# Optimization experiments

Hardware: AMD Instinct MI355X
Metric: run time of the kernel (lower is better)

The kernel has to match this reference:

```python
import jax, jax.numpy as jnp
import numpy as np

VOCAB, D, PATCH, ROUNDS = 256, 64, 4, 3
B, T = 32, 8192


def setup_inputs() -> dict:
    key = jax.random.key(0)
    ks = jax.random.split(key, 16)
    s = 0.02
    inp = {
        "x": jax.random.randint(ks[0], (B, T), 0, VOCAB),
        "emb": jax.random.normal(ks[1], (VOCAB, D), jnp.float32) * s,
        # msg_net: Linear(2d->d), GELU, Linear(d->d); weights stored [in, out]
        "w_m1": jax.random.normal(ks[2], (2 * D, D), jnp.float32) * s,
        "b_m1": jnp.zeros((D,), jnp.float32),
        "w_m2": jax.random.normal(ks[3], (D, D), jnp.float32) * s,
        "b_m2": jnp.zeros((D,), jnp.float32),
        # update_net: Linear(2d->d), GELU, Linear(d->d)
        "w_u1": jax.random.normal(ks[4], (2 * D, D), jnp.float32) * s,
        "b_u1": jnp.zeros((D,), jnp.float32),
        "w_u2": jax.random.normal(ks[5], (D, D), jnp.float32) * s,
        "b_u2": jnp.zeros((D,), jnp.float32),
        # LayerNorm(d)
        "ln_g": jnp.ones((D,), jnp.float32),
        "ln_b": jnp.zeros((D,), jnp.float32),
        # readout: Linear(d -> vocab)
        "w_r": jax.random.normal(ks[6], (D, VOCAB), jnp.float32) * s,
        "b_r": jnp.zeros((VOCAB,), jnp.float32),
    }
    return inp


def _mlp(z, w1, b1, w2, b2):
    h = jax.nn.gelu(z @ w1 + b1, approximate=False)  # torch nn.GELU default = exact erf
    return h @ w2 + b2


def _layernorm(h, g, b, eps=1e-5):
    mu = jnp.mean(h, axis=-1, keepdims=True)
    var = jnp.mean((h - mu) ** 2, axis=-1, keepdims=True)
    return (h - mu) / jnp.sqrt(var + eps) * g + b


def reference(x, emb, w_m1, b_m1, w_m2, b_m2, w_u1, b_u1, w_u2, b_u2, ln_g, ln_b, w_r, b_r):
    Bx, Tx = x.shape
    P = PATCH
    N = (Tx + P - 1) // P
    xp = jnp.pad(x, ((0, 0), (0, N * P - Tx)))  # pad token id 0
    h = emb[xp].reshape(Bx, N, P, D).mean(axis=2)  # [B, N, d] patch-node features
    for _ in range(ROUNDS):
        left = jnp.pad(h[:, :-1], ((0, 0), (1, 0), (0, 0)))  # shift-right along N
        msgs = _mlp(jnp.concatenate([h, left], axis=-1), w_m1, b_m1, w_m2, b_m2)
        upd = _mlp(jnp.concatenate([h, msgs], axis=-1), w_u1, b_u1, w_u2, b_u2)
        h = _layernorm(h + upd, ln_g, ln_b)
    tok = jnp.repeat(h, P, axis=1)[:, :Tx]  # broadcast node feat to its P tokens
    return tok @ w_r + b_r  # [B, T, vocab]
```

## Files before the change

kernel.cpp:

```cpp
#include <hip/hip_runtime.h>
#include <hip/hip_bf16.h>
#include <math.h>

#define DD 64
#define NPB 2048
#define RTOT 65536

typedef __bf16 bf16;
typedef bf16 bf16x8 __attribute__((ext_vector_type(8)));
typedef float f32x4 __attribute__((ext_vector_type(4)));
typedef short short4v __attribute__((ext_vector_type(4)));

#define COMPILER_FENCE() asm volatile("" ::: "memory")

__device__ __forceinline__ f32x4 mfma16(bf16x8 a, bf16x8 b, f32x4 c) {
  return __builtin_amdgcn_mfma_f32_16x16x32_bf16(a, b, c, 0, 0, 0);
}

__device__ __forceinline__ float gelu_fast(float x) {
  float u = fabsf(x) * 0.70710678118654752f;
  float t = __builtin_amdgcn_rcpf(fmaf(0.3275911f, u, 1.0f));
  float p = t * fmaf(t, fmaf(t, fmaf(t, fmaf(t, 1.061405429f, -1.453152027f),
                                     1.421413741f), -0.284496736f), 0.254829592f);
  float e = __expf(-u * u);
  float erfa = fmaf(-p, e, 1.0f);
  float s = copysignf(erfa, x);
  return 0.5f * x * (1.0f + s);
}

__device__ __forceinline__ int swz(int col, int row) {
  return col ^ ((row & 7) << 3);
}

__device__ __forceinline__ bf16x8 ld8(const bf16* p) {
  return *reinterpret_cast<const bf16x8*>(p);
}

__global__ void __launch_bounds__(256) k_pe(const int* __restrict__ x,
                                            const float* __restrict__ emb,
                                            const float* __restrict__ wm1,
                                            const float* __restrict__ wm2,
                                            const float* __restrict__ wu1,
                                            const float* __restrict__ wu2,
                                            const float* __restrict__ wr,
                                            bf16* __restrict__ Wsc,
                                            bf16* __restrict__ h) {
  const int b = blockIdx.x;
  if (b < 160) {
    int gid = b * 256 + threadIdx.x;
    if (gid < 8192) {
      int n = gid >> 7, k = gid & 127;
      Wsc[gid] = (bf16)wm1[k * 64 + n];
    } else if (gid < 16384) {
      int j = gid - 8192, n = j >> 7, k = j & 127;
      Wsc[gid] = (bf16)wu1[k * 64 + n];
    } else if (gid < 20480) {
      int j = gid - 16384, n = j >> 6, k = j & 63;
      Wsc[gid] = (bf16)wm2[k * 64 + n];
    } else if (gid < 24576) {
      int j = gid - 20480, n = j >> 6, k = j & 63;
      Wsc[gid] = (bf16)wu2[k * 64 + n];
    } else {
      int j = gid - 24576, v = j >> 6, k = j & 63;
      Wsc[gid] = (bf16)wr[k * 256 + v];
    }
  } else {
    int gid = (b - 160) * 256 + threadIdx.x;
    int row = gid >> 4, d0 = (gid & 15) * 4;
    const int* xp = x + row * 4;
    f32x4 s = {0.f, 0.f, 0.f, 0.f};
#pragma unroll
    for (int p = 0; p < 4; ++p)
      s += *reinterpret_cast<const f32x4*>(emb + xp[p] * DD + d0);
    short4v o;
#pragma unroll
    for (int j = 0; j < 4; ++j)
      o[j] = (short)__builtin_bit_cast(unsigned short, (bf16)(s[j] * 0.25f));
    *reinterpret_cast<short4v*>(h + row * DD + d0) = o;
  }
}

__global__ void __launch_bounds__(256) k_r(const bf16* __restrict__ hin,
                                           bf16* __restrict__ hout,
                                           const bf16* __restrict__ Wsc,
                                           const float* __restrict__ bm1,
                                           const float* __restrict__ bm2,
                                           const float* __restrict__ bu1,
                                           const float* __restrict__ bu2,
                                           const float* __restrict__ lng,
                                           const float* __restrict__ lnb) {
  __shared__ bf16 W1[2][64 * 128];
  __shared__ bf16 Ms[64 * 64];
  __shared__ bf16 Hs[64 * 64];

  const int tid = threadIdx.x;
  const int lane = tid & 63;
  const int wv = tid >> 6;
  const int l15 = lane & 15;
  const int lhi = lane >> 4;

  for (int i = tid; i < 2048; i += 256) {
    int buf = i >> 10, idx = i & 1023;
    int n = idx >> 4, g = (idx & 15) * 8;
    *reinterpret_cast<bf16x8*>(&W1[buf][n * 128 + swz(g, n)]) =
        ld8(Wsc + buf * 8192 + n * 128 + g);
  }
  bf16x8 fm2[4][2], fu2[4][2];
#pragma unroll
  for (int ct = 0; ct < 4; ++ct)
#pragma unroll
    for (int kt = 0; kt < 2; ++kt) {
      int off = (ct * 16 + l15) * 64 + kt * 32 + lhi * 8;
      fm2[ct][kt] = ld8(Wsc + 16384 + off);
      fu2[ct][kt] = ld8(Wsc + 20480 + off);
    }
  float bm1v[4], bm2v[4], bu1v[4], bu2v[4], lngv[4], lnbv[4];
#pragma unroll
  for (int ct = 0; ct < 4; ++ct) {
    int c = ct * 16 + l15;
    bm1v[ct] = bm1[c]; bm2v[ct] = bm2[c];
    bu1v[ct] = bu1[c]; bu2v[ct] = bu2[c];
    lngv[ct] = lng[c]; lnbv[ct] = lnb[c];
  }
  __syncthreads();

  const int lrow = wv * 16 + l15;
  const int sxr = (lrow & 7) << 3;
  const int sxw = (l15 & 7) << 3;
  const f32x4 fz = {0.f, 0.f, 0.f, 0.f};

  for (int tt = 0; tt < 2; ++tt) {
    const int rowbase = (blockIdx.x * 2 + tt) * 64;
    const int grow = rowbase + lrow;
    const bf16* hrow = hin + (size_t)grow * DD;

    bf16x8 ah0 = ld8(hrow + lhi * 8);
    bf16x8 ah1 = ld8(hrow + 32 + lhi * 8);
    bf16x8 al0, al1;
#pragma unroll
    for (int j = 0; j < 8; ++j) { al0[j] = (bf16)0.f; al1[j] = (bf16)0.f; }
    if ((grow & (NPB - 1)) != 0) {
      al0 = ld8(hrow - DD + lhi * 8);
      al1 = ld8(hrow - DD + 32 + lhi * 8);
    }

    f32x4 acc[4];
#pragma unroll
    for (int ct = 0; ct < 4; ++ct) acc[ct] = fz;
#pragma unroll
    for (int ct = 0; ct < 4; ++ct) {
      const bf16* wb = &W1[0][(ct * 16 + l15) * 128];
      acc[ct] = mfma16(ah0, ld8(wb + ((lhi * 8) ^ sxw)), acc[ct]);
      acc[ct] = mfma16(ah1, ld8(wb + ((32 + lhi * 8) ^ sxw)), acc[ct]);
      acc[ct] = mfma16(al0, ld8(wb + ((64 + lhi * 8) ^ sxw)), acc[ct]);
      acc[ct] = mfma16(al1, ld8(wb + ((96 + lhi * 8) ^ sxw)), acc[ct]);
    }
#pragma unroll
    for (int ct = 0; ct < 4; ++ct)
#pragma unroll
      for (int r = 0; r < 4; ++r) {
        float g = gelu_fast(acc[ct][r] + bm1v[ct]);
        int row = wv * 16 + lhi * 4 + r;
        Hs[row * 64 + swz(ct * 16 + l15, row)] = (bf16)g;
      }
    COMPILER_FENCE();
#pragma unroll
    for (int ct = 0; ct < 4; ++ct) acc[ct] = fz;
    {
      bf16x8 g0 = ld8(&Hs[lrow * 64 + ((lhi * 8) ^ sxr)]);
      bf16x8 g1 = ld8(&Hs[lrow * 64 + ((32 + lhi * 8) ^ sxr)]);
#pragma unroll
      for (int ct = 0; ct < 4; ++ct) {
        acc[ct] = mfma16(g0, fm2[ct][0], acc[ct]);
        acc[ct] = mfma16(g1, fm2[ct][1], acc[ct]);
      }
    }
#pragma unroll
    for (int ct = 0; ct < 4; ++ct)
#pragma unroll
      for (int r = 0; r < 4; ++r) {
        int row = wv * 16 + lhi * 4 + r;
        Ms[row * 64 + swz(ct * 16 + l15, row)] = (bf16)(acc[ct][r] + bm2v[ct]);
      }
    COMPILER_FENCE();
#pragma unroll
    for (int ct = 0; ct < 4; ++ct) acc[ct] = fz;
    {
      bf16x8 m0 = ld8(&Ms[lrow * 64 + ((lhi * 8) ^ sxr)]);
      bf16x8 m1 = ld8(&Ms[lrow * 64 + ((32 + lhi * 8) ^ sxr)]);
#pragma unroll
      for (int ct = 0; ct < 4; ++ct) {
        const bf16* wb = &W1[1][(ct * 16 + l15) * 128];
        acc[ct] = mfma16(ah0, ld8(wb + ((lhi * 8) ^ sxw)), acc[ct]);
        acc[ct] = mfma16(ah1, ld8(wb + ((32 + lhi * 8) ^ sxw)), acc[ct]);
        acc[ct] = mfma16(m0, ld8(wb + ((64 + lhi * 8) ^ sxw)), acc[ct]);
        acc[ct] = mfma16(m1, ld8(wb + ((96 + lhi * 8) ^ sxw)), acc[ct]);
      }
    }
    COMPILER_FENCE();
#pragma unroll
    for (int ct = 0; ct < 4; ++ct)
#pragma unroll
      for (int r = 0; r < 4; ++r) {
        float g = gelu_fast(acc[ct][r] + bu1v[ct]);
        int row = wv * 16 + lhi * 4 + r;
        Hs[row * 64 + swz(ct * 16 + l15, row)] = (bf16)g;
      }
    COMPILER_FENCE();
#pragma unroll
    for (int ct = 0; ct < 4; ++ct) acc[ct] = fz;
    {
      bf16x8 u0 = ld8(&Hs[lrow * 64 + ((lhi * 8) ^ sxr)]);
      bf16x8 u1 = ld8(&Hs[lrow * 64 + ((32 + lhi * 8) ^ sxr)]);
#pragma unroll
      for (int ct = 0; ct < 4; ++ct) {
        acc[ct] = mfma16(u0, fu2[ct][0], acc[ct]);
        acc[ct] = mfma16(u1, fu2[ct][1], acc[ct]);
      }
    }
    float xv[4][4];
#pragma unroll
    for (int ct = 0; ct < 4; ++ct)
#pragma unroll
      for (int r = 0; r < 4; ++r) {
        int row = rowbase + wv * 16 + lhi * 4 + r;
        xv[ct][r] = acc[ct][r] + bu2v[ct] + (float)hin[(size_t)row * DD + ct * 16 + l15];
      }
    float s1[4], s2[4];
#pragma unroll
    for (int r = 0; r < 4; ++r) {
      s1[r] = 0.f; s2[r] = 0.f;
#pragma unroll
      for (int ct = 0; ct < 4; ++ct) { s1[r] += xv[ct][r]; s2[r] += xv[ct][r] * xv[ct][r]; }
    }
#pragma unroll
    for (int off = 1; off < 16; off <<= 1)
#pragma unroll
      for (int r = 0; r < 4; ++r) {
        s1[r] += __shfl_xor(s1[r], off);
        s2[r] += __shfl_xor(s2[r], off);
      }
#pragma unroll
    for (int r = 0; r < 4; ++r) {
      float mu = s1[r] * 0.015625f;
      float var = s2[r] * 0.015625f - mu * mu;
      float rstd = rsqrtf(var + 1e-5f);
      int row = rowbase + wv * 16 + lhi * 4 + r;
#pragma unroll
      for (int ct = 0; ct < 4; ++ct)
        hout[(size_t)row * DD + ct * 16 + l15] =
            (bf16)((xv[ct][r] - mu) * rstd * lngv[ct] + lnbv[ct]);
    }
  }
}

__global__ void __launch_bounds__(256) k_r3r(const bf16* __restrict__ hin,
                                             const bf16* __restrict__ Wsc,
                                             const float* __restrict__ bm1,
                                             const float* __restrict__ bm2,
                                             const float* __restrict__ bu1,
                                             const float* __restrict__ bu2,
                                             const float* __restrict__ lng,
                                             const float* __restrict__ lnb,
                                             const float* __restrict__ br,
                                             float* __restrict__ out) {
  __shared__ bf16 W1[2][64 * 128];
  __shared__ bf16 Ms[64 * 64];
  __shared__ bf16 Hs[64 * 64];

  const int tid = threadIdx.x;
  const int lane = tid & 63;
  const int wv = tid >> 6;
  const int l15 = lane & 15;
  const int lhi = lane >> 4;

  for (int i = tid; i < 2048; i += 256) {
    int buf = i >> 10, idx = i & 1023;
    int n = idx >> 4, g = (idx & 15) * 8;
    *reinterpret_cast<bf16x8*>(&W1[buf][n * 128 + swz(g, n)]) =
        ld8(Wsc + buf * 8192 + n * 128 + g);
  }
  bf16x8 fm2[4][2], fu2[4][2];
#pragma unroll
  for (int ct = 0; ct < 4; ++ct)
#pragma unroll
    for (int kt = 0; kt < 2; ++kt) {
      int off = (ct * 16 + l15) * 64 + kt * 32 + lhi * 8;
      fm2[ct][kt] = ld8(Wsc + 16384 + off);
      fu2[ct][kt] = ld8(Wsc + 20480 + off);
    }
  const bf16* wrt = Wsc + 24576;
  float bm1v[4], bm2v[4], bu1v[4], bu2v[4], lngv[4], lnbv[4];
#pragma unroll
  for (int ct = 0; ct < 4; ++ct) {
    int c = ct * 16 + l15;
    bm1v[ct] = bm1[c]; bm2v[ct] = bm2[c];
    bu1v[ct] = bu1[c]; bu2v[ct] = bu2[c];
    lngv[ct] = lng[c]; lnbv[ct] = lnb[c];
  }
  __syncthreads();

  const int lrow = wv * 16 + l15;
  const int sxr = (lrow & 7) << 3;
  const int sxw = (l15 & 7) << 3;
  const f32x4 fz = {0.f, 0.f, 0.f, 0.f};

  for (int tt = 0; tt < 2; ++tt) {
    const int rowbase = (blockIdx.x * 2 + tt) * 64;
    const int grow = rowbase + lrow;
    const bf16* hrow = hin + (size_t)grow * DD;

    bf16x8 ah0 = ld8(hrow + lhi * 8);
    bf16x8 ah1 = ld8(hrow + 32 + lhi * 8);
    bf16x8 al0, al1;
#pragma unroll
    for (int j = 0; j < 8; ++j) { al0[j] = (bf16)0.f; al1[j] = (bf16)0.f; }
    if ((grow & (NPB - 1)) != 0) {
      al0 = ld8(hrow - DD + lhi * 8);
      al1 = ld8(hrow - DD + 32 + lhi * 8);
    }

    f32x4 acc[4];
#pragma unroll
    for (int ct = 0; ct < 4; ++ct) acc[ct] = fz;
#pragma unroll
    for (int ct = 0; ct < 4; ++ct) {
      const bf16* wb = &W1[0][(ct * 16 + l15) * 128];
      acc[ct] = mfma16(ah0, ld8(wb + ((lhi * 8) ^ sxw)), acc[ct]);
      acc[ct] = mfma16(ah1, ld8(wb + ((32 + lhi * 8) ^ sxw)), acc[ct]);
      acc[ct] = mfma16(al0, ld8(wb + ((64 + lhi * 8) ^ sxw)), acc[ct]);
      acc[ct] = mfma16(al1, ld8(wb + ((96 + lhi * 8) ^ sxw)), acc[ct]);
    }
#pragma unroll
    for (int ct = 0; ct < 4; ++ct)
#pragma unroll
      for (int r = 0; r < 4; ++r) {
        float g = gelu_fast(acc[ct][r] + bm1v[ct]);
        int row = wv * 16 + lhi * 4 + r;
        Hs[row * 64 + swz(ct * 16 + l15, row)] = (bf16)g;
      }
    COMPILER_FENCE();
#pragma unroll
    for (int ct = 0; ct < 4; ++ct) acc[ct] = fz;
    {
      bf16x8 g0 = ld8(&Hs[lrow * 64 + ((lhi * 8) ^ sxr)]);
      bf16x8 g1 = ld8(&Hs[lrow * 64 + ((32 + lhi * 8) ^ sxr)]);
#pragma unroll
      for (int ct = 0; ct < 4; ++ct) {
        acc[ct] = mfma16(g0, fm2[ct][0], acc[ct]);
        acc[ct] = mfma16(g1, fm2[ct][1], acc[ct]);
      }
    }
#pragma unroll
    for (int ct = 0; ct < 4; ++ct)
#pragma unroll
      for (int r = 0; r < 4; ++r) {
        int row = wv * 16 + lhi * 4 + r;
        Ms[row * 64 + swz(ct * 16 + l15, row)] = (bf16)(acc[ct][r] + bm2v[ct]);
      }
    COMPILER_FENCE();
#pragma unroll
    for (int ct = 0; ct < 4; ++ct) acc[ct] = fz;
    {
      bf16x8 m0 = ld8(&Ms[lrow * 64 + ((lhi * 8) ^ sxr)]);
      bf16x8 m1 = ld8(&Ms[lrow * 64 + ((32 + lhi * 8) ^ sxr)]);
#pragma unroll
      for (int ct = 0; ct < 4; ++ct) {
        const bf16* wb = &W1[1][(ct * 16 + l15) * 128];
        acc[ct] = mfma16(ah0, ld8(wb + ((lhi * 8) ^ sxw)), acc[ct]);
        acc[ct] = mfma16(ah1, ld8(wb + ((32 + lhi * 8) ^ sxw)), acc[ct]);
        acc[ct] = mfma16(m0, ld8(wb + ((64 + lhi * 8) ^ sxw)), acc[ct]);
        acc[ct] = mfma16(m1, ld8(wb + ((96 + lhi * 8) ^ sxw)), acc[ct]);
      }
    }
    COMPILER_FENCE();
#pragma unroll
    for (int ct = 0; ct < 4; ++ct)
#pragma unroll
      for (int r = 0; r < 4; ++r) {
        float g = gelu_fast(acc[ct][r] + bu1v[ct]);
        int row = wv * 16 + lhi * 4 + r;
        Hs[row * 64 + swz(ct * 16 + l15, row)] = (bf16)g;
      }
    COMPILER_FENCE();
#pragma unroll
    for (int ct = 0; ct < 4; ++ct) acc[ct] = fz;
    {
      bf16x8 u0 = ld8(&Hs[lrow * 64 + ((lhi * 8) ^ sxr)]);
      bf16x8 u1 = ld8(&Hs[lrow * 64 + ((32 + lhi * 8) ^ sxr)]);
#pragma unroll
      for (int ct = 0; ct < 4; ++ct) {
        acc[ct] = mfma16(u0, fu2[ct][0], acc[ct]);
        acc[ct] = mfma16(u1, fu2[ct][1], acc[ct]);
      }
    }
    float xv[4][4];
#pragma unroll
    for (int ct = 0; ct < 4; ++ct)
#pragma unroll
      for (int r = 0; r < 4; ++r) {
        int row = rowbase + wv * 16 + lhi * 4 + r;
        xv[ct][r] = acc[ct][r] + bu2v[ct] + (float)hin[(size_t)row * DD + ct * 16 + l15];
      }
    float s1[4], s2[4];
#pragma unroll
    for (int r = 0; r < 4; ++r) {
      s1[r] = 0.f; s2[r] = 0.f;
#pragma unroll
      for (int ct = 0; ct < 4; ++ct) { s1[r] += xv[ct][r]; s2[r] += xv[ct][r] * xv[ct][r]; }
    }
#pragma unroll
    for (int off = 1; off < 16; off <<= 1)
#pragma unroll
      for (int r = 0; r < 4; ++r) {
        s1[r] += __shfl_xor(s1[r], off);
        s2[r] += __shfl_xor(s2[r], off);
      }
#pragma unroll
    for (int r = 0; r < 4; ++r) {
      float mu = s1[r] * 0.015625f;
      float var = s2[r] * 0.015625f - mu * mu;
      float rstd = rsqrtf(var + 1e-5f);
      int row = wv * 16 + lhi * 4 + r;
#pragma unroll
      for (int ct = 0; ct < 4; ++ct)
        Ms[row * 64 + swz(ct * 16 + l15, row)] =
            (bf16)((xv[ct][r] - mu) * rstd * lngv[ct] + lnbv[ct]);
    }
    COMPILER_FENCE();

    {
      bf16x8 b0 = ld8(&Ms[lrow * 64 + ((lhi * 8) ^ sxr)]);
      bf16x8 b1 = ld8(&Ms[lrow * 64 + ((32 + lhi * 8) ^ sxr)]);
      const int node = rowbase + lrow;
      float* ob = out + (size_t)node * 1024 + lhi * 4;
#pragma unroll
      for (int vt = 0; vt < 16; ++vt) {
        const bf16* wb = wrt + (vt * 16 + l15) * 64;
        f32x4 a = mfma16(ld8(wb + lhi * 8), b0, fz);
        a = mfma16(ld8(wb + 32 + lhi * 8), b1, a);
        f32x4 val = a + *reinterpret_cast<const f32x4*>(br + vt * 16 + lhi * 4);
        float* p = ob + vt * 16;
#pragma unroll
        for (int rep = 0; rep < 4; ++rep)
          *reinterpret_cast<f32x4*>(p + rep * 256) = val;
      }
    }
    COMPILER_FENCE();
  }
}

extern "C" void kernel_launch(void* const* d_in, const int* in_sizes, int n_in,
                              void* d_out, int out_size, void* d_ws, size_t ws_size,
                              hipStream_t stream) {
  const int*   x   = (const int*)d_in[0];
  const float* emb = (const float*)d_in[1];
  const float* wm1 = (const float*)d_in[2];
  const float* bm1 = (const float*)d_in[3];
  const float* wm2 = (const float*)d_in[4];
  const float* bm2 = (const float*)d_in[5];
  const float* wu1 = (const float*)d_in[6];
  const float* bu1 = (const float*)d_in[7];
  const float* wu2 = (const float*)d_in[8];
  const float* bu2 = (const float*)d_in[9];
  const float* lng = (const float*)d_in[10];
  const float* lnb = (const float*)d_in[11];
  const float* wr  = (const float*)d_in[12];
  const float* br  = (const float*)d_in[13];
  float* out = (float*)d_out;

  char* ws = (char*)d_ws;
  bf16* hA  = (bf16*)ws;
  bf16* hB  = (bf16*)(ws + (size_t)RTOT * DD * 2);
  bf16* Wsc = (bf16*)(ws + (size_t)RTOT * DD * 4);

  hipLaunchKernelGGL(k_pe, dim3(4256), dim3(256), 0, stream,
                     x, emb, wm1, wm2, wu1, wu2, wr, Wsc, hA);
  hipLaunchKernelGGL(k_r, dim3(512), dim3(256), 0, stream,
                     hA, hB, Wsc, bm1, bm2, bu1, bu2, lng, lnb);
  hipLaunchKernelGGL(k_r, dim3(512), dim3(256), 0, stream,
                     hB, hA, Wsc, bm1, bm2, bu1, bu2, lng, lnb);
  hipLaunchKernelGGL(k_r3r, dim3(512), dim3(256), 0, stream,
                     hA, Wsc, bm1, bm2, bu1, bu2, lng, lnb, br, out);
}
```

Measured before the change: 116.1 us.

## Stage readout weights in LDS, prefetch next tile inputs, fold bias into MFMA

The readout weight matrix (256x64 bf16) is copied once per block into swizzled shared memory rather than read from global memory inside the readout loop. The readout bias is preloaded into registers and used as the initial MFMA accumulator, which removes a separate add and load. The second tile's node and residual inputs are loaded during the first tile's readout so their latency overlaps with the output stores. In exchange the block uses 32KB more LDS, which may reduce occupancy, and holds more registers for the prefetched data.

After: 112.1 us, median of 2. 3.4% less time.

```diff
diff --git a/kernel.cpp b/kernel.cpp
--- a/kernel.cpp
+++ b/kernel.cpp
@@ -267,6 +267,7 @@
   __shared__ bf16 W1[2][64 * 128];
   __shared__ bf16 Ms[64 * 64];
   __shared__ bf16 Hs[64 * 64];
+  __shared__ bf16 Wt[256 * 64];
 
   const int tid = threadIdx.x;
   const int lane = tid & 63;
@@ -280,6 +281,13 @@
     *reinterpret_cast<bf16x8*>(&W1[buf][n * 128 + swz(g, n)]) =
         ld8(Wsc + buf * 8192 + n * 128 + g);
   }
+  {
+    const bf16* wrt = Wsc + 24576;
+    for (int i = tid; i < 2048; i += 256) {
+      int v = i >> 3, g = (i & 7) * 8;
+      *reinterpret_cast<bf16x8*>(&Wt[v * 64 + swz(g, v)]) = ld8(wrt + v * 64 + g);
+    }
+  }
   bf16x8 fm2[4][2], fu2[4][2];
 #pragma unroll
   for (int ct = 0; ct < 4; ++ct)
@@ -289,7 +297,6 @@
       fm2[ct][kt] = ld8(Wsc + 16384 + off);
       fu2[ct][kt] = ld8(Wsc + 20480 + off);
     }
-  const bf16* wrt = Wsc + 24576;
   float bm1v[4], bm2v[4], bu1v[4], bu2v[4], lngv[4], lnbv[4];
 #pragma unroll
   for (int ct = 0; ct < 4; ++ct) {
@@ -298,26 +305,39 @@
     bu1v[ct] = bu1[c]; bu2v[ct] = bu2[c];
     lngv[ct] = lng[c]; lnbv[ct] = lnb[c];
   }
+  f32x4 brv[16];
+#pragma unroll
+  for (int vt = 0; vt < 16; ++vt)
+    brv[vt] = *reinterpret_cast<const f32x4*>(br + vt * 16 + lhi * 4);
   __syncthreads();
 
   const int lrow = wv * 16 + l15;
   const int sxr = (lrow & 7) << 3;
   const int sxw = (l15 & 7) << 3;
+  const int sxv = (l15 & 7) << 3;
   const f32x4 fz = {0.f, 0.f, 0.f, 0.f};
 
+  bf16x8 pah0, pah1, pal0, pal1;
+  float pres[4][4];
+
+#pragma unroll
   for (int tt = 0; tt < 2; ++tt) {
     const int rowbase = (blockIdx.x * 2 + tt) * 64;
     const int grow = rowbase + lrow;
     const bf16* hrow = hin + (size_t)grow * DD;
 
-    bf16x8 ah0 = ld8(hrow + lhi * 8);
-    bf16x8 ah1 = ld8(hrow + 32 + lhi * 8);
-    bf16x8 al0, al1;
-#pragma unroll
-    for (int j = 0; j < 8; ++j) { al0[j] = (bf16)0.f; al1[j] = (bf16)0.f; }
-    if ((grow & (NPB - 1)) != 0) {
-      al0 = ld8(hrow - DD + lhi * 8);
-      al1 = ld8(hrow - DD + 32 + lhi * 8);
+    bf16x8 ah0, ah1, al0, al1;
+    if (tt == 0) {
+      ah0 = ld8(hrow + lhi * 8);
+      ah1 = ld8(hrow + 32 + lhi * 8);
+#pragma unroll
+      for (int j = 0; j < 8; ++j) { al0[j] = (bf16)0.f; al1[j] = (bf16)0.f; }
+      if ((grow & (NPB - 1)) != 0) {
+        al0 = ld8(hrow - DD + lhi * 8);
+        al1 = ld8(hrow - DD + 32 + lhi * 8);
+      }
+    } else {
+      ah0 = pah0; ah1 = pah1; al0 = pal0; al1 = pal1;
     }
 
     f32x4 acc[4];
@@ -399,8 +419,12 @@
     for (int ct = 0; ct < 4; ++ct)
 #pragma unroll
       for (int r = 0; r < 4; ++r) {
-        int row = rowbase + wv * 16 + lhi * 4 + r;
-        xv[ct][r] = acc[ct][r] + bu2v[ct] + (float)hin[(size_t)row * DD + ct * 16 + l15];
+        if (tt == 0) {
+          int row = rowbase + wv * 16 + lhi * 4 + r;
+          xv[ct][r] = acc[ct][r] + bu2v[ct] + (float)hin[(size_t)row * DD + ct * 16 + l15];
+        } else {
+          xv[ct][r] = acc[ct][r] + bu2v[ct] + pres[ct][r];
+        }
       }
     float s1[4], s2[4];
 #pragma unroll
@@ -429,6 +453,26 @@
     }
     COMPILER_FENCE();
 
+    if (tt == 0) {
+      const int grow1 = grow + 64;
+      const bf16* hrow1 = hin + (size_t)grow1 * DD;
+      pah0 = ld8(hrow1 + lhi * 8);
+      pah1 = ld8(hrow1 + 32 + lhi * 8);
+#pragma unroll
+      for (int j = 0; j < 8; ++j) { pal0[j] = (bf16)0.f; pal1[j] = (bf16)0.f; }
+      if ((grow1 & (NPB - 1)) != 0) {
+        pal0 = ld8(hrow1 - DD + lhi * 8);
+        pal1 = ld8(hrow1 - DD + 32 + lhi * 8);
+      }
+#pragma unroll
+      for (int ct = 0; ct < 4; ++ct)
+#pragma unroll
+        for (int r = 0; r < 4; ++r) {
+          int row = rowbase + 64 + wv * 16 + lhi * 4 + r;
+          pres[ct][r] = (float)hin[(size_t)row * DD + ct * 16 + l15];
+        }
+    }
+
     {
       bf16x8 b0 = ld8(&Ms[lrow * 64 + ((lhi * 8) ^ sxr)]);
       bf16x8 b1 = ld8(&Ms[lrow * 64 + ((32 + lhi * 8) ^ sxr)]);
@@ -436,14 +480,15 @@
       float* ob = out + (size_t)node * 1024 + lhi * 4;
 #pragma unroll
       for (int vt = 0; vt < 16; ++vt) {
-        const bf16* wb = wrt + (vt * 16 + l15) * 64;
-        f32x4 a = mfma16(ld8(wb + lhi * 8), b0, fz);
-        a = mfma16(ld8(wb + 32 + lhi * 8), b1, a);
-        f32x4 val = a + *reinterpret_cast<const f32x4*>(br + vt * 16 + lhi * 4);
+        const bf16* wb = &Wt[(vt * 16 + l15) * 64];
+        bf16x8 a0 = ld8(wb + ((lhi * 8) ^ sxv));
+        bf16x8 a1 = ld8(wb + ((32 + lhi * 8) ^ sxv));
+        f32x4 a = mfma16(a0, b0, brv[vt]);
+        a = mfma16(a1, b1, a);
         float* p = ob + vt * 16;
 #pragma unroll
         for (int rep = 0; rep < 4; ++rep)
-          *reinterpret_cast<f32x4*>(p + rep * 256) = val;
+          *reinterpret_cast<f32x4*>(p + rep * 256) = a;
       }
     }
     COMPILER_FENCE();
```
